# Kernel tuning notes

Measured on AMD Instinct MI355X. Metric: run time of the kernel, lower is better.

The kernel has to match this reference:

```python
import jax, jax.numpy as jnp
import numpy as np
import math

N = 4096
D = 256
H = 8
DH = D // H
E_RAND = 131072
EPS = 1e-5


def _layernorm(x, g, b):
    mu = jnp.mean(x, axis=-1, keepdims=True)
    var = jnp.mean((x - mu) ** 2, axis=-1, keepdims=True)
    return (x - mu) * jax.lax.rsqrt(var + EPS) * g + b


def setup_inputs() -> dict:
    key = jax.random.key(0)
    ks = jax.random.split(key, 16)
    s = 1.0 / math.sqrt(D)
    x = jax.random.normal(ks[0], (N, D), dtype=jnp.float32)
    src = jax.random.randint(ks[1], (E_RAND,), 0, N)
    dst = jax.random.randint(ks[2], (E_RAND,), 0, N)
    loop = jnp.arange(N)
    edge_index = jnp.stack([jnp.concatenate([src, loop]),
                            jnp.concatenate([dst, loop])]).astype(jnp.int64)
    def lin(k):
        return jax.random.normal(k, (D, D), dtype=jnp.float32) * s
    return {
        "x": x,
        "edge_index": edge_index,
        "Wq": lin(ks[3]), "bq": jnp.zeros((D,), jnp.float32),
        "Wk": lin(ks[4]), "bk": jnp.zeros((D,), jnp.float32),
        "Wv": lin(ks[5]), "bv": jnp.zeros((D,), jnp.float32),
        "Wo": lin(ks[6]), "bo": jnp.zeros((D,), jnp.float32),
        "g1": jnp.ones((D,), jnp.float32), "b1": jnp.zeros((D,), jnp.float32),
        "g2": jnp.ones((D,), jnp.float32), "b2": jnp.zeros((D,), jnp.float32),
        "Wm1": jax.random.normal(ks[7], (D, 2 * D), jnp.float32) * s,
        "bm1": jnp.zeros((2 * D,), jnp.float32),
        "Wm2": jax.random.normal(ks[8], (2 * D, D), jnp.float32) * (1.0 / math.sqrt(2 * D)),
        "bm2": jnp.zeros((D,), jnp.float32),
    }


def reference(x, edge_index, Wq, bq, Wk, bk, Wv, bv, Wo, bo,
              g1, b1, g2, b2, Wm1, bm1, Wm2, bm2):
    scale = 1.0 / math.sqrt(DH)
    h = _layernorm(x, g1, b1)
    # [N, D] -> [H, N, DH]
    q = (h @ Wq + bq).reshape(N, H, DH).transpose(1, 0, 2)
    k = (h @ Wk + bk).reshape(N, H, DH).transpose(1, 0, 2)
    v = (h @ Wv + bv).reshape(N, H, DH).transpose(1, 0, 2)
    att = jnp.einsum('hnd,hmd->hnm', q, k) * scale  # [H, N, N]
    # mask: True everywhere except edges (edge positions are attended)
    mask = jnp.ones((N, N), dtype=bool).at[edge_index[0], edge_index[1]].set(False)
    att = jnp.where(mask[None, :, :], -jnp.inf, att)
    att = jax.nn.softmax(att, axis=-1)
    y = jnp.einsum('hnm,hmd->hnd', att, v)  # [H, N, DH]
    y = y.transpose(1, 0, 2).reshape(N, D)
    x = x + (y @ Wo + bo)
    h2 = _layernorm(x, g2, b2)
    x = x + (jax.nn.gelu(h2 @ Wm1 + bm1, approximate=False) @ Wm2 + bm2)
    return x
```

## Files before the change

kernel.cpp:

```cpp
#include <hip/hip_runtime.h>
#include <hip/hip_bf16.h>

#define N_NODES 4096
#define D_MODEL 256
#define NWORDS 128
#define CAP 96

typedef __attribute__((ext_vector_type(8))) short short8;
typedef __attribute__((ext_vector_type(4))) short short4v;
typedef __attribute__((ext_vector_type(4))) float f32x4;

__device__ __forceinline__ unsigned short f2b(float f) {
    unsigned u = __float_as_uint(f);
    return (unsigned short)((u + 0x7FFFu + ((u >> 16) & 1u)) >> 16);
}
__device__ __forceinline__ float b2f(unsigned short u) {
    return __uint_as_float((unsigned)u << 16);
}

__global__ __launch_bounds__(256) void prep_kernel(const float* __restrict__ Wq,
        const float* __restrict__ Wk, const float* __restrict__ Wv,
        const float* __restrict__ Wo, const float* __restrict__ Wm1,
        const float* __restrict__ Wm2, unsigned short* __restrict__ wbf,
        uint4* __restrict__ bitmap, const int* __restrict__ ei,
        int* __restrict__ flag, const float* __restrict__ x,
        const float* __restrict__ g1, const float* __restrict__ b1,
        unsigned short* __restrict__ h) {
    int b = blockIdx.x, t = threadIdx.x;
    if (b < 2048) {
        int e = b * 256 + t;
        const float* W; int base, K, M;
        if (e < 262144) {
            int r = e >> 16;
            W = (r == 0) ? Wq : (r == 1) ? Wk : (r == 2) ? Wv : Wo;
            base = r << 16; K = 256; M = 256;
        } else if (e < 393216) { W = Wm1; base = 262144; K = 256; M = 512; }
        else                   { W = Wm2; base = 393216; K = 512; M = 256; }
        int i = e - base;
        int m = i / K, k = i - m * K;
        wbf[e] = f2b(W[k * M + m]);
    } else if (b < 2560) {
        bitmap[(size_t)(b - 2048) * 256 + t] = uint4{0, 0, 0, 0};
    } else if (b == 2560) {
        if (t == 0) {
            int is64 = 1;
            for (int i = 1; i < 128; i += 2)
                if (ei[i] != 0) { is64 = 0; break; }
            *flag = is64;
        }
    } else {
        int row = b - 2561;
        float v = x[row * D_MODEL + t];
        __shared__ float red[4];
        float s = v;
        #pragma unroll
        for (int off = 32; off; off >>= 1) s += __shfl_down(s, off, 64);
        if ((t & 63) == 0) red[t >> 6] = s;
        __syncthreads();
        float mu = (red[0] + red[1] + red[2] + red[3]) * (1.0f / 256.0f);
        __syncthreads();
        float d = v - mu;
        float s2 = d * d;
        #pragma unroll
        for (int off = 32; off; off >>= 1) s2 += __shfl_down(s2, off, 64);
        if ((t & 63) == 0) red[t >> 6] = s2;
        __syncthreads();
        float var = (red[0] + red[1] + red[2] + red[3]) * (1.0f / 256.0f);
        h[row * D_MODEL + t] = f2b(d * rsqrtf(var + 1e-5f) * g1[t] + b1[t]);
    }
}

template <int K, int MODE, bool LNA, bool STATS>
__global__ __launch_bounds__(512) void gemm_bf16(const unsigned short* __restrict__ A,
        const float* __restrict__ Af, const float* __restrict__ psum,
        const float* __restrict__ psum2, const float* __restrict__ lng,
        const float* __restrict__ lnb, const unsigned short* __restrict__ BT,
        const float* __restrict__ bias, const float* __restrict__ bias_k,
        const float* __restrict__ bias_v, const float* __restrict__ R,
        float* __restrict__ Cf, unsigned short* __restrict__ Cb,
        unsigned short* __restrict__ Ck, unsigned short* __restrict__ Cv,
        float* __restrict__ opsum, float* __restrict__ opsum2, int M,
        const int* __restrict__ ei, int E, const int* __restrict__ flag,
        unsigned* __restrict__ bitmap, int nadj) {
    int tid = threadIdx.x;
    if (MODE == 3 && (int)blockIdx.x < nadj) {
        int e = (int)blockIdx.x * 512 + tid;
        if (e < E) {
            int n, m;
            if (*flag) { n = ei[2 * e]; m = ei[2 * (E + e)]; }
            else       { n = ei[e];     m = ei[E + e]; }
            atomicOr(&bitmap[n * NWORDS + (m >> 5)], 1u << (m & 31));
        }
        return;
    }
    __shared__ unsigned short Asm[64][72];
    __shared__ unsigned short Bsm[64][72];
    __shared__ float psA[64][2], psA2[64][2];
    __shared__ float muS[64], invS[64];

    int bx2  = (MODE == 3) ? ((int)blockIdx.x - nadj) : 0;
    int brow = (MODE == 3) ? ((bx2 & 63) << 6) : ((int)blockIdx.x << 6);
    int by   = (MODE == 3) ? (bx2 >> 6) : (int)blockIdx.y;
    int bcol = by << 6;
    int wid = tid >> 6, lane = tid & 63;
    int wr = wid >> 1, wc = wid & 1;
    int l15 = lane & 15, lhi = lane >> 4;
    int r0 = tid >> 3, c0 = (tid & 7) << 3;

    float mu_r = 0.f, inv_r = 0.f;
    if (LNA) {
        if (tid < 64) {
            float4 s4 = ((const float4*)psum)[brow + tid];
            float4 q4 = ((const float4*)psum2)[brow + tid];
            float S  = s4.x + s4.y + s4.z + s4.w;
            float S2 = q4.x + q4.y + q4.z + q4.w;
            float mu = S * (1.0f / 256.0f);
            muS[tid] = mu;
            invS[tid] = rsqrtf(S2 * (1.0f / 256.0f) - mu * mu + 1e-5f);
        }
        __syncthreads();
        mu_r = muS[r0]; inv_r = invS[r0];
    }

    const unsigned short* Bp = BT + (size_t)(bcol + r0) * K + c0;
    f32x4 acc[2] = {};
    short8 areg;
    float4 xa, xb, ga, gb, ba, bb;
    if (LNA) {
        const float* Xp = Af + (size_t)(brow + r0) * 256 + c0;
        xa = *(const float4*)(Xp);
        xb = *(const float4*)(Xp + 4);
        ga = *(const float4*)(lng + c0); gb = *(const float4*)(lng + c0 + 4);
        ba = *(const float4*)(lnb + c0); bb = *(const float4*)(lnb + c0 + 4);
    } else {
        areg = *(const short8*)(A + (size_t)(brow + r0) * K + c0);
    }
    short8 breg = *(const short8*)(Bp);

    #pragma unroll
    for (int k0 = 0; k0 < K; k0 += 64) {
        if (LNA) {
            float xv[8] = {xa.x, xa.y, xa.z, xa.w, xb.x, xb.y, xb.z, xb.w};
            float gv[8] = {ga.x, ga.y, ga.z, ga.w, gb.x, gb.y, gb.z, gb.w};
            float bv[8] = {ba.x, ba.y, ba.z, ba.w, bb.x, bb.y, bb.z, bb.w};
            short8 o;
            #pragma unroll
            for (int j = 0; j < 8; ++j)
                o[j] = (short)f2b((xv[j] - mu_r) * inv_r * gv[j] + bv[j]);
            *(short8*)&Asm[r0][c0] = o;
        } else {
            *(short8*)&Asm[r0][c0] = areg;
        }
        *(short8*)&Bsm[r0][c0] = breg;
        __syncthreads();
        if (k0 + 64 < K) {
            if (LNA) {
                const float* Xp = Af + (size_t)(brow + r0) * 256 + k0 + 64 + c0;
                xa = *(const float4*)(Xp);
                xb = *(const float4*)(Xp + 4);
                ga = *(const float4*)(lng + k0 + 64 + c0);
                gb = *(const float4*)(lng + k0 + 64 + c0 + 4);
                ba = *(const float4*)(lnb + k0 + 64 + c0);
                bb = *(const float4*)(lnb + k0 + 64 + c0 + 4);
            } else {
                areg = *(const short8*)(A + (size_t)(brow + r0) * K + k0 + 64 + c0);
            }
            breg = *(const short8*)(Bp + k0 + 64);
        }
        #pragma unroll
        for (int ks = 0; ks < 2; ++ks) {
            int kc = ks * 32 + lhi * 8;
            short8 a_0 = *(const short8*)&Asm[wr * 16 + l15][kc];
            short8 b_0 = *(const short8*)&Bsm[wc * 32 + l15][kc];
            short8 b_1 = *(const short8*)&Bsm[wc * 32 + 16 + l15][kc];
            acc[0] = __builtin_amdgcn_mfma_f32_16x16x32_bf16(a_0, b_0, acc[0], 0, 0, 0);
            acc[1] = __builtin_amdgcn_mfma_f32_16x16x32_bf16(a_0, b_1, acc[1], 0, 0, 0);
        }
        __syncthreads();
    }

    float cs[2][4];
    #pragma unroll
    for (int sn = 0; sn < 2; ++sn) {
        int col = bcol + wc * 32 + sn * 16 + l15;
        float bs;
        if (MODE == 3)
            bs = (col < 256) ? bias[col]
               : (col < 512) ? bias_k[col - 256] : bias_v[col - 512];
        else
            bs = bias[col];
        #pragma unroll
        for (int r = 0; r < 4; ++r) {
            int row = brow + wr * 16 + lhi * 4 + r;
            float c = acc[sn][r] + bs;
            if (MODE == 1) {
                c = 0.5f * c * (1.0f + erff(c * 0.70710678118654752f));
                Cb[(size_t)row * M + col] = f2b(c);
            } else if (MODE == 2) {
                c += R[(size_t)row * M + col];
                Cf[(size_t)row * M + col] = c;
            } else if (MODE == 3) {
                int part = col >> 8, cc = col & 255;
                unsigned short* dst = (part == 0) ? Cb : (part == 1) ? Ck : Cv;
                dst[(((size_t)(cc >> 5) * N_NODES + row) << 5) + (cc & 31)] = f2b(c);
            } else {
                Cb[(size_t)row * M + col] = f2b(c);
            }
            if (STATS) cs[sn][r] = c;
        }
    }
    if (STATS) {
        #pragma unroll
        for (int r = 0; r < 4; ++r) {
            float s  = cs[0][r] + cs[1][r];
            float s2 = cs[0][r] * cs[0][r] + cs[1][r] * cs[1][r];
            #pragma unroll
            for (int off = 1; off < 16; off <<= 1) {
                s  += __shfl_xor(s, off, 64);
                s2 += __shfl_xor(s2, off, 64);
            }
            if (l15 == 0) {
                int rl = wr * 16 + lhi * 4 + r;
                psA[rl][wc] = s; psA2[rl][wc] = s2;
            }
        }
        __syncthreads();
        if (tid < 64) {
            opsum [(size_t)(brow + tid) * 4 + by] = psA[tid][0] + psA[tid][1];
            opsum2[(size_t)(brow + tid) * 4 + by] = psA2[tid][0] + psA2[tid][1];
        }
    }
}

#define TRLOAD(dst_, OFF_) \
    asm volatile("ds_read_b64_tr_b16 %0, %1 offset:" #OFF_ \
                 : "=v"(dst_) : "v"(trbase))
#define PVSTEP(tv_, b_) { \
    float4 pv = *(const float4*)&pArr[g][4 * (b_)]; \
    acc = fmaf(pv.x, b2f((unsigned short)tv_[0]), acc); \
    acc = fmaf(pv.y, b2f((unsigned short)tv_[1]), acc); \
    acc = fmaf(pv.z, b2f((unsigned short)tv_[2]), acc); \
    acc = fmaf(pv.w, b2f((unsigned short)tv_[3]), acc); }

__global__ __launch_bounds__(256) void attn_kernel(const unsigned short* __restrict__ qh,
        const unsigned short* __restrict__ kh, const unsigned short* __restrict__ vh,
        const unsigned* __restrict__ bitmap, unsigned short* __restrict__ y) {
    int bid = blockIdx.x, tid = threadIdx.x;
    int h = bid & 7, oct = bid >> 3;
    int g = tid >> 5, lane = tid & 31;
    int n = oct * 8 + g;
    __shared__ int sIdx[8][CAP];
    __shared__ unsigned short Vst[8][2176];
    __shared__ float pArr[8][64];

    const unsigned short* qp = qh + (((size_t)h * N_NODES + n) << 5);
    float qreg[32];
    #pragma unroll
    for (int i = 0; i < 4; ++i) {
        short8 q8 = *(const short8*)(qp + i * 8);
        #pragma unroll
        for (int j = 0; j < 8; ++j) qreg[i * 8 + j] = b2f((unsigned short)q8[j]);
    }

    uint4 w4 = ((const uint4*)(bitmap + (size_t)n * NWORDS))[lane];
    unsigned words[4] = {w4.x, w4.y, w4.z, w4.w};
    int pc = __popc(w4.x) + __popc(w4.y) + __popc(w4.z) + __popc(w4.w);
    int pre = pc;
    #pragma unroll
    for (int off = 1; off < 32; off <<= 1) {
        int u = __shfl_up(pre, off, 32);
        if (lane >= off) pre += u;
    }
    int c = __shfl(pre, 31, 32);
    int off = pre - pc;
    #pragma unroll
    for (int i = 0; i < 4; ++i) {
        unsigned word = words[i];
        int wbase = ((lane << 2) + i) << 5;
        while (word) {
            int bit = __ffs(word) - 1;
            word &= word - 1;
            if (off < CAP) sIdx[g][off] = wbase + bit;
            ++off;
        }
    }
    c = min(c, CAP);
    for (int i = c + lane; i < 64; i += 32) sIdx[g][i] = 0;
    __syncthreads();

    int idx_a = sIdx[g][lane], idx_b = sIdx[g][lane + 32];
    const size_t hb = (size_t)h * N_NODES << 5;

    const unsigned short* va = vh + hb + ((size_t)idx_a << 5);
    const unsigned short* vb = vh + hb + ((size_t)idx_b << 5);
    short8 va0 = *(const short8*)(va);      short8 va1 = *(const short8*)(va + 8);
    short8 va2 = *(const short8*)(va + 16); short8 va3 = *(const short8*)(va + 24);
    short8 vb0 = *(const short8*)(vb);      short8 vb1 = *(const short8*)(vb + 8);
    short8 vb2 = *(const short8*)(vb + 16); short8 vb3 = *(const short8*)(vb + 24);

    const unsigned short* ka = kh + hb + ((size_t)idx_a << 5);
    const unsigned short* kb = kh + hb + ((size_t)idx_b << 5);
    short8 ka0 = *(const short8*)(ka);      short8 ka1 = *(const short8*)(ka + 8);
    short8 ka2 = *(const short8*)(ka + 16); short8 ka3 = *(const short8*)(ka + 24);
    short8 kb0 = *(const short8*)(kb);      short8 kb1 = *(const short8*)(kb + 8);
    short8 kb2 = *(const short8*)(kb + 16); short8 kb3 = *(const short8*)(kb + 24);

    {
        unsigned short* vr = &Vst[g][(lane >> 2) * 136 + (lane & 3) * 16];
        *(short8*)(vr + 0)  = va0;
        *(short8*)(vr + 8)  = va1;
        *(short8*)(vr + 64) = va2;
        *(short8*)(vr + 72) = va3;
        unsigned short* vr2 = vr + 8 * 136;
        *(short8*)(vr2 + 0)  = vb0;
        *(short8*)(vr2 + 8)  = vb1;
        *(short8*)(vr2 + 64) = vb2;
        *(short8*)(vr2 + 72) = vb3;
    }

    float da0 = 0.f, da1 = 0.f, db0 = 0.f, db1 = 0.f;
    #pragma unroll
    for (int e = 0; e < 8; ++e) {
        da0 = fmaf(qreg[e],      b2f((unsigned short)ka0[e]), da0);
        da1 = fmaf(qreg[8 + e],  b2f((unsigned short)ka1[e]), da1);
        da0 = fmaf(qreg[16 + e], b2f((unsigned short)ka2[e]), da0);
        da1 = fmaf(qreg[24 + e], b2f((unsigned short)ka3[e]), da1);
        db0 = fmaf(qreg[e],      b2f((unsigned short)kb0[e]), db0);
        db1 = fmaf(qreg[8 + e],  b2f((unsigned short)kb1[e]), db1);
        db0 = fmaf(qreg[16 + e], b2f((unsigned short)kb2[e]), db0);
        db1 = fmaf(qreg[24 + e], b2f((unsigned short)kb3[e]), db1);
    }
    const float sc = 0.17677669529663687f;
    float s_a = (lane < c)      ? (da0 + da1) * sc : -INFINITY;
    float s_b = (lane + 32 < c) ? (db0 + db1) * sc : -INFINITY;

    float bm = fmaxf(s_a, s_b);
    #pragma unroll
    for (int o2 = 16; o2; o2 >>= 1) bm = fmaxf(bm, __shfl_xor(bm, o2, 32));
    float p_a = (lane < c)      ? __expf(s_a - bm) : 0.0f;
    float p_b = (lane + 32 < c) ? __expf(s_b - bm) : 0.0f;
    float S = p_a + p_b;
    #pragma unroll
    for (int o2 = 16; o2; o2 >>= 1) S += __shfl_xor(S, o2, 32);
    pArr[g][lane] = p_a;
    pArr[g][lane + 32] = p_b;

    unsigned trbase = (unsigned)(uintptr_t)(&Vst[g][0])
                    + ((unsigned)(lane >> 4) << 7) + ((unsigned)(lane & 15) << 3);
    asm volatile("s_waitcnt lgkmcnt(0)" ::: "memory");
    short4v t0, t1, t2, t3, t4, t5, t6, t7, t8, t9, t10, t11, t12, t13, t14, t15;
    TRLOAD(t0, 0);     TRLOAD(t1, 272);  TRLOAD(t2, 544);  TRLOAD(t3, 816);
    TRLOAD(t4, 1088);  TRLOAD(t5, 1360); TRLOAD(t6, 1632); TRLOAD(t7, 1904);
    TRLOAD(t8, 2176);  TRLOAD(t9, 2448); TRLOAD(t10, 2720); TRLOAD(t11, 2992);
    TRLOAD(t12, 3264); TRLOAD(t13, 3536); TRLOAD(t14, 3808); TRLOAD(t15, 4080);
    asm volatile("s_waitcnt lgkmcnt(0)" ::: "memory");
    __builtin_amdgcn_sched_barrier(0);

    float acc = 0.0f;
    PVSTEP(t0, 0)   PVSTEP(t1, 1)   PVSTEP(t2, 2)   PVSTEP(t3, 3)
    PVSTEP(t4, 4)   PVSTEP(t5, 5)   PVSTEP(t6, 6)   PVSTEP(t7, 7)
    PVSTEP(t8, 8)   PVSTEP(t9, 9)   PVSTEP(t10, 10) PVSTEP(t11, 11)
    PVSTEP(t12, 12) PVSTEP(t13, 13) PVSTEP(t14, 14) PVSTEP(t15, 15)

    if (c > 64) {
        float m_run = bm;
        for (int b0 = 64; b0 < c; b0 += 32) {
            int j = b0 + lane;
            float s = -INFINITY;
            if (j < c) {
                const unsigned short* kp = kh + hb + ((size_t)sIdx[g][j] << 5);
                float d = 0.0f;
                #pragma unroll
                for (int i = 0; i < 4; ++i) {
                    short8 k8 = *(const short8*)(kp + i * 8);
                    #pragma unroll
                    for (int e = 0; e < 8; ++e)
                        d = fmaf(qreg[i * 8 + e], b2f((unsigned short)k8[e]), d);
                }
                s = d * sc;
            }
            float bm2 = s;
            #pragma unroll
            for (int o2 = 16; o2; o2 >>= 1) bm2 = fmaxf(bm2, __shfl_xor(bm2, o2, 32));
            float newM = fmaxf(m_run, bm2);
            float p = (j < c) ? __expf(s - newM) : 0.0f;
            float bs = p;
            #pragma unroll
            for (int o2 = 16; o2; o2 >>= 1) bs += __shfl_xor(bs, o2, 32);
            float scale = __expf(m_run - newM);
            S = S * scale + bs;
            acc *= scale;
            int lim = min(32, c - b0);
            const unsigned short* vbase = vh + hb + lane;
            for (int jj = 0; jj < lim; ++jj) {
                float pj = __shfl(p, jj, 32);
                acc = fmaf(pj, b2f(vbase[(size_t)sIdx[g][b0 + jj] << 5]), acc);
            }
            m_run = newM;
        }
    }
    y[(size_t)n * 256 + h * 32 + lane] = f2b(acc / S);
}

extern "C" void kernel_launch(void* const* d_in, const int* in_sizes, int n_in,
                              void* d_out, int out_size, void* d_ws, size_t ws_size,
                              hipStream_t stream) {
    const float* x   = (const float*)d_in[0];
    const int*   ei  = (const int*)d_in[1];
    const float* Wq  = (const float*)d_in[2];  const float* bq  = (const float*)d_in[3];
    const float* Wk  = (const float*)d_in[4];  const float* bk  = (const float*)d_in[5];
    const float* Wv  = (const float*)d_in[6];  const float* bv  = (const float*)d_in[7];
    const float* Wo  = (const float*)d_in[8];  const float* bo  = (const float*)d_in[9];
    const float* g1  = (const float*)d_in[10]; const float* b1  = (const float*)d_in[11];
    const float* g2  = (const float*)d_in[12]; const float* b2  = (const float*)d_in[13];
    const float* Wm1 = (const float*)d_in[14]; const float* bm1 = (const float*)d_in[15];
    const float* Wm2 = (const float*)d_in[16]; const float* bm2 = (const float*)d_in[17];
    float* out = (float*)d_out;
    int E = in_sizes[1] / 2;
    int nadj = (E + 511) / 512;

    char* WS = (char*)d_ws;
    const size_t MB = 1u << 20;
    unsigned*       bitmap = (unsigned*)WS;
    int*            flag   = (int*)(WS + 2 * MB);
    float*          psum   = (float*)(WS + 2 * MB + 4096);
    float*          psum2  = (float*)(WS + 2 * MB + 4096 + 65536);
    unsigned short* wbf    = (unsigned short*)(WS + 3 * MB);
    unsigned short* y      = (unsigned short*)(WS + 4 * MB);
    float*          x1     = (float*)(WS + 6 * MB);
    unsigned short* m1     = (unsigned short*)(WS + 10 * MB);
    unsigned short* h      = (unsigned short*)(WS + 14 * MB);
    unsigned short* qh     = (unsigned short*)(WS + 16 * MB);
    unsigned short* kh     = (unsigned short*)(WS + 18 * MB);
    unsigned short* vh     = (unsigned short*)(WS + 20 * MB);

    const unsigned short* WTqkv = wbf;
    const unsigned short* WTo   = wbf + 196608;
    const unsigned short* WTm1  = wbf + 262144;
    const unsigned short* WTm2  = wbf + 393216;

    prep_kernel<<<6657, 256, 0, stream>>>(Wq, Wk, Wv, Wo, Wm1, Wm2, wbf,
                                          (uint4*)bitmap, ei, flag, x, g1, b1, h);
    gemm_bf16<256, 3, false, false><<<nadj + 768, 512, 0, stream>>>(h, nullptr,
            nullptr, nullptr, nullptr, nullptr, WTqkv, bq, bk, bv, nullptr,
            nullptr, qh, kh, vh, nullptr, nullptr, 768, ei, E, flag, bitmap, nadj);
    attn_kernel<<<N_NODES, 256, 0, stream>>>(qh, kh, vh, bitmap, y);
    gemm_bf16<256, 2, false, true><<<dim3(64, 4), 512, 0, stream>>>(y, nullptr,
            nullptr, nullptr, nullptr, nullptr, WTo, bo, nullptr, nullptr, x,
            x1, nullptr, nullptr, nullptr, psum, psum2, 256, nullptr, 0, nullptr, nullptr, 0);
    gemm_bf16<256, 1, true, false><<<dim3(64, 8), 512, 0, stream>>>(nullptr, x1,
            psum, psum2, g2, b2, WTm1, bm1, nullptr, nullptr, nullptr,
            nullptr, m1, nullptr, nullptr, nullptr, nullptr, 512, nullptr, 0, nullptr, nullptr, 0);
    gemm_bf16<512, 2, false, false><<<dim3(64, 4), 512, 0, stream>>>(m1, nullptr,
            nullptr, nullptr, nullptr, nullptr, WTm2, bm2, nullptr, nullptr, x1,
            out, nullptr, nullptr, nullptr, nullptr, nullptr, 256, nullptr, 0, nullptr, nullptr, 0);
}
```

Baseline: 70.30 us.

## Tile weight transpose via LDS, add BM=128 GEMM tiles, prescale V by probabilities

Weight conversion now transposes 64x64 tiles through shared memory with coalesced float4 reads and short8 writes, replacing the strided per-element gather. The GEMM gains a BM template parameter, and the QKV and MLP1 launches use 128-row tiles so each B tile is reused across twice as many rows, with half as many blocks. In attention, V rows are multiplied by their softmax probability and packed back to bf16 before the transposed LDS reads, so the P·V step becomes plain sums. This drops the pArr shared buffer but rounds p*v to bf16, adding a small precision loss.

```diff
diff --git a/kernel.cpp b/kernel.cpp
--- a/kernel.cpp
+++ b/kernel.cpp
@@ -16,6 +16,19 @@
 }
 __device__ __forceinline__ float b2f(unsigned short u) {
     return __uint_as_float((unsigned)u << 16);
+}
+__device__ __forceinline__ unsigned pk2(float lo, float hi) {
+    unsigned r;
+    asm("v_cvt_pk_bf16_f32 %0, %1, %2" : "=v"(r) : "v"(lo), "v"(hi));
+    return r;
+}
+__device__ __forceinline__ uint4 scale8(short8 v, float p) {
+    uint4 r;
+    r.x = pk2(b2f((unsigned short)v[0]) * p, b2f((unsigned short)v[1]) * p);
+    r.y = pk2(b2f((unsigned short)v[2]) * p, b2f((unsigned short)v[3]) * p);
+    r.z = pk2(b2f((unsigned short)v[4]) * p, b2f((unsigned short)v[5]) * p);
+    r.w = pk2(b2f((unsigned short)v[6]) * p, b2f((unsigned short)v[7]) * p);
+    return r;
 }
 
 __global__ __launch_bounds__(256) void prep_kernel(const float* __restrict__ Wq,
@@ -27,21 +40,34 @@
         const float* __restrict__ g1, const float* __restrict__ b1,
         unsigned short* __restrict__ h) {
     int b = blockIdx.x, t = threadIdx.x;
-    if (b < 2048) {
-        int e = b * 256 + t;
-        const float* W; int base, K, M;
-        if (e < 262144) {
-            int r = e >> 16;
-            W = (r == 0) ? Wq : (r == 1) ? Wk : (r == 2) ? Wv : Wo;
-            base = r << 16; K = 256; M = 256;
-        } else if (e < 393216) { W = Wm1; base = 262144; K = 256; M = 512; }
-        else                   { W = Wm2; base = 393216; K = 512; M = 256; }
-        int i = e - base;
-        int m = i / K, k = i - m * K;
-        wbf[e] = f2b(W[k * M + m]);
-    } else if (b < 2560) {
-        bitmap[(size_t)(b - 2048) * 256 + t] = uint4{0, 0, 0, 0};
-    } else if (b == 2560) {
+    if (b < 128) {
+        const float* W; int base, K, M, kt, mt;
+        if (b < 64)      { int r = b >> 4; W = (r == 0) ? Wq : (r == 1) ? Wk : (r == 2) ? Wv : Wo;
+                           base = r << 16; K = 256; M = 256; kt = (b & 15) >> 2; mt = b & 3; }
+        else if (b < 96) { W = Wm1; base = 262144; K = 256; M = 512; kt = (b - 64) >> 3; mt = (b - 64) & 7; }
+        else             { W = Wm2; base = 393216; K = 512; M = 256; kt = (b - 96) >> 2; mt = (b - 96) & 3; }
+        __shared__ unsigned short Lt[64][66];
+        #pragma unroll
+        for (int i = 0; i < 4; ++i) {
+            int lin = i * 256 + t;
+            int r = lin >> 4, c4 = (lin & 15) << 2;
+            float4 v = *(const float4*)&W[(size_t)(kt * 64 + r) * M + mt * 64 + c4];
+            Lt[r][c4 + 0] = f2b(v.x); Lt[r][c4 + 1] = f2b(v.y);
+            Lt[r][c4 + 2] = f2b(v.z); Lt[r][c4 + 3] = f2b(v.w);
+        }
+        __syncthreads();
+        #pragma unroll
+        for (int i = 0; i < 2; ++i) {
+            int lin = i * 256 + t;
+            int mr = lin >> 3, kc = (lin & 7) << 3;
+            short8 o;
+            #pragma unroll
+            for (int e = 0; e < 8; ++e) o[e] = (short)Lt[kc + e][mr];
+            *(short8*)&wbf[base + (size_t)(mt * 64 + mr) * K + kt * 64 + kc] = o;
+        }
+    } else if (b < 640) {
+        bitmap[(size_t)(b - 128) * 256 + t] = uint4{0, 0, 0, 0};
+    } else if (b == 640) {
         if (t == 0) {
             int is64 = 1;
             for (int i = 1; i < 128; i += 2)
@@ -49,7 +75,7 @@
             *flag = is64;
         }
     } else {
-        int row = b - 2561;
+        int row = b - 641;
         float v = x[row * D_MODEL + t];
         __shared__ float red[4];
         float s = v;
@@ -70,7 +96,7 @@
     }
 }
 
-template <int K, int MODE, bool LNA, bool STATS>
+template <int K, int BM, int MODE, bool LNA, bool STATS>
 __global__ __launch_bounds__(512) void gemm_bf16(const unsigned short* __restrict__ A,
         const float* __restrict__ Af, const float* __restrict__ psum,
         const float* __restrict__ psum2, const float* __restrict__ lng,
@@ -82,6 +108,8 @@
         float* __restrict__ opsum, float* __restrict__ opsum2, int M,
         const int* __restrict__ ei, int E, const int* __restrict__ flag,
         unsigned* __restrict__ bitmap, int nadj) {
+    constexpr int MR = BM / 64;
+    constexpr int NRB = 4096 / BM;
     int tid = threadIdx.x;
     if (MODE == 3 && (int)blockIdx.x < nadj) {
         int e = (int)blockIdx.x * 512 + tid;
@@ -93,23 +121,23 @@
         }
         return;
     }
-    __shared__ unsigned short Asm[64][72];
+    __shared__ unsigned short Asm[BM][72];
     __shared__ unsigned short Bsm[64][72];
     __shared__ float psA[64][2], psA2[64][2];
-    __shared__ float muS[64], invS[64];
+    __shared__ float muS[BM], invS[BM];
 
     int bx2  = (MODE == 3) ? ((int)blockIdx.x - nadj) : 0;
-    int brow = (MODE == 3) ? ((bx2 & 63) << 6) : ((int)blockIdx.x << 6);
-    int by   = (MODE == 3) ? (bx2 >> 6) : (int)blockIdx.y;
+    int brow = (MODE == 3) ? ((bx2 % NRB) * BM) : ((int)blockIdx.x * BM);
+    int by   = (MODE == 3) ? (bx2 / NRB) : (int)blockIdx.y;
     int bcol = by << 6;
     int wid = tid >> 6, lane = tid & 63;
     int wr = wid >> 1, wc = wid & 1;
     int l15 = lane & 15, lhi = lane >> 4;
     int r0 = tid >> 3, c0 = (tid & 7) << 3;
 
-    float mu_r = 0.f, inv_r = 0.f;
+    float mu_r[MR], inv_r[MR];
     if (LNA) {
-        if (tid < 64) {
+        if (tid < BM) {
             float4 s4 = ((const float4*)psum)[brow + tid];
             float4 q4 = ((const float4*)psum2)[brow + tid];
             float S  = s4.x + s4.y + s4.z + s4.w;
@@ -119,96 +147,118 @@
             invS[tid] = rsqrtf(S2 * (1.0f / 256.0f) - mu * mu + 1e-5f);
         }
         __syncthreads();
-        mu_r = muS[r0]; inv_r = invS[r0];
+        #pragma unroll
+        for (int m = 0; m < MR; ++m) { mu_r[m] = muS[r0 + m * 64]; inv_r[m] = invS[r0 + m * 64]; }
     }
 
     const unsigned short* Bp = BT + (size_t)(bcol + r0) * K + c0;
-    f32x4 acc[2] = {};
-    short8 areg;
-    float4 xa, xb, ga, gb, ba, bb;
+    f32x4 acc[MR][2] = {};
+    short8 areg[MR];
+    float4 xa[MR], xb[MR], ga, gb, ba, bb;
     if (LNA) {
-        const float* Xp = Af + (size_t)(brow + r0) * 256 + c0;
-        xa = *(const float4*)(Xp);
-        xb = *(const float4*)(Xp + 4);
+        #pragma unroll
+        for (int m = 0; m < MR; ++m) {
+            const float* Xp = Af + (size_t)(brow + r0 + m * 64) * 256 + c0;
+            xa[m] = *(const float4*)(Xp);
+            xb[m] = *(const float4*)(Xp + 4);
+        }
         ga = *(const float4*)(lng + c0); gb = *(const float4*)(lng + c0 + 4);
         ba = *(const float4*)(lnb + c0); bb = *(const float4*)(lnb + c0 + 4);
     } else {
-        areg = *(const short8*)(A + (size_t)(brow + r0) * K + c0);
+        #pragma unroll
+        for (int m = 0; m < MR; ++m)
+            areg[m] = *(const short8*)(A + (size_t)(brow + r0 + m * 64) * K + c0);
     }
     short8 breg = *(const short8*)(Bp);
 
     #pragma unroll
     for (int k0 = 0; k0 < K; k0 += 64) {
         if (LNA) {
-            float xv[8] = {xa.x, xa.y, xa.z, xa.w, xb.x, xb.y, xb.z, xb.w};
-            float gv[8] = {ga.x, ga.y, ga.z, ga.w, gb.x, gb.y, gb.z, gb.w};
-            float bv[8] = {ba.x, ba.y, ba.z, ba.w, bb.x, bb.y, bb.z, bb.w};
-            short8 o;
-            #pragma unroll
-            for (int j = 0; j < 8; ++j)
-                o[j] = (short)f2b((xv[j] - mu_r) * inv_r * gv[j] + bv[j]);
-            *(short8*)&Asm[r0][c0] = o;
+            #pragma unroll
+            for (int m = 0; m < MR; ++m) {
+                float xv[8] = {xa[m].x, xa[m].y, xa[m].z, xa[m].w,
+                               xb[m].x, xb[m].y, xb[m].z, xb[m].w};
+                float gv[8] = {ga.x, ga.y, ga.z, ga.w, gb.x, gb.y, gb.z, gb.w};
+                float bv[8] = {ba.x, ba.y, ba.z, ba.w, bb.x, bb.y, bb.z, bb.w};
+                short8 o;
+                #pragma unroll
+                for (int j = 0; j < 8; ++j)
+                    o[j] = (short)f2b((xv[j] - mu_r[m]) * inv_r[m] * gv[j] + bv[j]);
+                *(short8*)&Asm[r0 + m * 64][c0] = o;
+            }
         } else {
-            *(short8*)&Asm[r0][c0] = areg;
+            #pragma unroll
+            for (int m = 0; m < MR; ++m)
+                *(short8*)&Asm[r0 + m * 64][c0] = areg[m];
         }
         *(short8*)&Bsm[r0][c0] = breg;
         __syncthreads();
         if (k0 + 64 < K) {
             if (LNA) {
-                const float* Xp = Af + (size_t)(brow + r0) * 256 + k0 + 64 + c0;
-                xa = *(const float4*)(Xp);
-                xb = *(const float4*)(Xp + 4);
+                #pragma unroll
+                for (int m = 0; m < MR; ++m) {
+                    const float* Xp = Af + (size_t)(brow + r0 + m * 64) * 256 + k0 + 64 + c0;
+                    xa[m] = *(const float4*)(Xp);
+                    xb[m] = *(const float4*)(Xp + 4);
+                }
                 ga = *(const float4*)(lng + k0 + 64 + c0);
                 gb = *(const float4*)(lng + k0 + 64 + c0 + 4);
                 ba = *(const float4*)(lnb + k0 + 64 + c0);
                 bb = *(const float4*)(lnb + k0 + 64 + c0 + 4);
             } else {
-                areg = *(const short8*)(A + (size_t)(brow + r0) * K + k0 + 64 + c0);
+                #pragma unroll
+                for (int m = 0; m < MR; ++m)
+                    areg[m] = *(const short8*)(A + (size_t)(brow + r0 + m * 64) * K + k0 + 64 + c0);
             }
             breg = *(const short8*)(Bp + k0 + 64);
         }
         #pragma unroll
         for (int ks = 0; ks < 2; ++ks) {
             int kc = ks * 32 + lhi * 8;
-            short8 a_0 = *(const short8*)&Asm[wr * 16 + l15][kc];
             short8 b_0 = *(const short8*)&Bsm[wc * 32 + l15][kc];
             short8 b_1 = *(const short8*)&Bsm[wc * 32 + 16 + l15][kc];
-            acc[0] = __builtin_amdgcn_mfma_f32_16x16x32_bf16(a_0, b_0, acc[0], 0, 0, 0);
-            acc[1] = __builtin_amdgcn_mfma_f32_16x16x32_bf16(a_0, b_1, acc[1], 0, 0, 0);
+            #pragma unroll
+            for (int sm = 0; sm < MR; ++sm) {
+                short8 a_s = *(const short8*)&Asm[wr * 16 * MR + sm * 16 + l15][kc];
+                acc[sm][0] = __builtin_amdgcn_mfma_f32_16x16x32_bf16(a_s, b_0, acc[sm][0], 0, 0, 0);
+                acc[sm][1] = __builtin_amdgcn_mfma_f32_16x16x32_bf16(a_s, b_1, acc[sm][1], 0, 0, 0);
+            }
         }
         __syncthreads();
     }
 
     float cs[2][4];
     #pragma unroll
-    for (int sn = 0; sn < 2; ++sn) {
-        int col = bcol + wc * 32 + sn * 16 + l15;
-        float bs;
-        if (MODE == 3)
-            bs = (col < 256) ? bias[col]
-               : (col < 512) ? bias_k[col - 256] : bias_v[col - 512];
-        else
-            bs = bias[col];
-        #pragma unroll
-        for (int r = 0; r < 4; ++r) {
-            int row = brow + wr * 16 + lhi * 4 + r;
-            float c = acc[sn][r] + bs;
-            if (MODE == 1) {
-                c = 0.5f * c * (1.0f + erff(c * 0.70710678118654752f));
-                Cb[(size_t)row * M + col] = f2b(c);
-            } else if (MODE == 2) {
-                c += R[(size_t)row * M + col];
-                Cf[(size_t)row * M + col] = c;
-            } else if (MODE == 3) {
-                int part = col >> 8, cc = col & 255;
-                unsigned short* dst = (part == 0) ? Cb : (part == 1) ? Ck : Cv;
-                dst[(((size_t)(cc >> 5) * N_NODES + row) << 5) + (cc & 31)] = f2b(c);
-            } else {
-                Cb[(size_t)row * M + col] = f2b(c);
-            }
-            if (STATS) cs[sn][r] = c;
-        }
-    }
+    for (int sm = 0; sm < MR; ++sm)
+        #pragma unroll
+        for (int sn = 0; sn < 2; ++sn) {
+            int col = bcol + wc * 32 + sn * 16 + l15;
+            float bs;
+            if (MODE == 3)
+                bs = (col < 256) ? bias[col]
+                   : (col < 512) ? bias_k[col - 256] : bias_v[col - 512];
+            else
+                bs = bias[col];
+            #pragma unroll
+            for (int r = 0; r < 4; ++r) {
+                int row = brow + wr * 16 * MR + sm * 16 + lhi * 4 + r;
+                float c = acc[sm][sn][r] + bs;
+                if (MODE == 1) {
+                    c = 0.5f * c * (1.0f + erff(c * 0.70710678118654752f));
+                    Cb[(size_t)row * M + col] = f2b(c);
+                } else if (MODE == 2) {
+                    c += R[(size_t)row * M + col];
+                    Cf[(size_t)row * M + col] = c;
+                } else if (MODE == 3) {
+                    int part = col >> 8, cc = col & 255;
+                    unsigned short* dst = (part == 0) ? Cb : (part == 1) ? Ck : Cv;
+                    dst[(((size_t)(cc >> 5) * N_NODES + row) << 5) + (cc & 31)] = f2b(c);
+                } else {
+                    Cb[(size_t)row * M + col] = f2b(c);
+                }
+                if (STATS) cs[sn][r] = c;
+            }
+        }
     if (STATS) {
         #pragma unroll
         for (int r = 0; r < 4; ++r) {
@@ -235,12 +285,9 @@
 #define TRLOAD(dst_, OFF_) \
     asm volatile("ds_read_b64_tr_b16 %0, %1 offset:" #OFF_ \
                  : "=v"(dst_) : "v"(trbase))
-#define PVSTEP(tv_, b_) { \
-    float4 pv = *(const float4*)&pArr[g][4 * (b_)]; \
-    acc = fmaf(pv.x, b2f((unsigned short)tv_[0]), acc); \
-    acc = fmaf(pv.y, b2f((unsigned short)tv_[1]), acc); \
-    acc = fmaf(pv.z, b2f((unsigned short)tv_[2]), acc); \
-    acc = fmaf(pv.w, b2f((unsigned short)tv_[3]), acc); }
+#define PVSUM(tv_) { \
+    acc0 += b2f((unsigned short)tv_[0]); acc1 += b2f((unsigned short)tv_[1]); \
+    acc0 += b2f((unsigned short)tv_[2]); acc1 += b2f((unsigned short)tv_[3]); }
 
 __global__ __launch_bounds__(256) void attn_kernel(const unsigned short* __restrict__ qh,
         const unsigned short* __restrict__ kh, const unsigned short* __restrict__ vh,
@@ -251,7 +298,6 @@
     int n = oct * 8 + g;
     __shared__ int sIdx[8][CAP];
     __shared__ unsigned short Vst[8][2176];
-    __shared__ float pArr[8][64];
 
     const unsigned short* qp = qh + (((size_t)h * N_NODES + n) << 5);
     float qreg[32];
@@ -304,19 +350,6 @@
     short8 ka2 = *(const short8*)(ka + 16); short8 ka3 = *(const short8*)(ka + 24);
     short8 kb0 = *(const short8*)(kb);      short8 kb1 = *(const short8*)(kb + 8);
     short8 kb2 = *(const short8*)(kb + 16); short8 kb3 = *(const short8*)(kb + 24);
-
-    {
-        unsigned short* vr = &Vst[g][(lane >> 2) * 136 + (lane & 3) * 16];
-        *(short8*)(vr + 0)  = va0;
-        *(short8*)(vr + 8)  = va1;
-        *(short8*)(vr + 64) = va2;
-        *(short8*)(vr + 72) = va3;
-        unsigned short* vr2 = vr + 8 * 136;
-        *(short8*)(vr2 + 0)  = vb0;
-        *(short8*)(vr2 + 8)  = vb1;
-        *(short8*)(vr2 + 64) = vb2;
-        *(short8*)(vr2 + 72) = vb3;
-    }
 
     float da0 = 0.f, da1 = 0.f, db0 = 0.f, db1 = 0.f;
     #pragma unroll
@@ -342,8 +375,19 @@
     float S = p_a + p_b;
     #pragma unroll
     for (int o2 = 16; o2; o2 >>= 1) S += __shfl_xor(S, o2, 32);
-    pArr[g][lane] = p_a;
-    pArr[g][lane + 32] = p_b;
+
+    {
+        unsigned short* vr = &Vst[g][(lane >> 2) * 136 + (lane & 3) * 16];
+        *(uint4*)(vr + 0)  = scale8(va0, p_a);
+        *(uint4*)(vr + 8)  = scale8(va1, p_a);
+        *(uint4*)(vr + 64) = scale8(va2, p_a);
+        *(uint4*)(vr + 72) = scale8(va3, p_a);
+        unsigned short* vr2 = vr + 8 * 136;
+        *(uint4*)(vr2 + 0)  = scale8(vb0, p_b);
+        *(uint4*)(vr2 + 8)  = scale8(vb1, p_b);
+        *(uint4*)(vr2 + 64) = scale8(vb2, p_b);
+        *(uint4*)(vr2 + 72) = scale8(vb3, p_b);
+    }
 
     unsigned trbase = (unsigned)(uintptr_t)(&Vst[g][0])
                     + ((unsigned)(lane >> 4) << 7) + ((unsigned)(lane & 15) << 3);
@@ -356,11 +400,12 @@
     asm volatile("s_waitcnt lgkmcnt(0)" ::: "memory");
     __builtin_amdgcn_sched_barrier(0);
 
-    float acc = 0.0f;
-    PVSTEP(t0, 0)   PVSTEP(t1, 1)   PVSTEP(t2, 2)   PVSTEP(t3, 3)
-    PVSTEP(t4, 4)   PVSTEP(t5, 5)   PVSTEP(t6, 6)   PVSTEP(t7, 7)
-    PVSTEP(t8, 8)   PVSTEP(t9, 9)   PVSTEP(t10, 10) PVSTEP(t11, 11)
-    PVSTEP(t12, 12) PVSTEP(t13, 13) PVSTEP(t14, 14) PVSTEP(t15, 15)
+    float acc0 = 0.0f, acc1 = 0.0f;
+    PVSUM(t0)  PVSUM(t1)  PVSUM(t2)  PVSUM(t3)
+    PVSUM(t4)  PVSUM(t5)  PVSUM(t6)  PVSUM(t7)
+    PVSUM(t8)  PVSUM(t9)  PVSUM(t10) PVSUM(t11)
+    PVSUM(t12) PVSUM(t13) PVSUM(t14) PVSUM(t15)
+    float acc = acc0 + acc1;
 
     if (c > 64) {
         float m_run = bm;
@@ -439,19 +484,19 @@
     const unsigned short* WTm1  = wbf + 262144;
     const unsigned short* WTm2  = wbf + 393216;
 
-    prep_kernel<<<6657, 256, 0, stream>>>(Wq, Wk, Wv, Wo, Wm1, Wm2, wbf,
+    prep_kernel<<<4737, 256, 0, stream>>>(Wq, Wk, Wv, Wo, Wm1, Wm2, wbf,
                                           (uint4*)bitmap, ei, flag, x, g1, b1, h);
-    gemm_bf16<256, 3, false, false><<<nadj + 768, 512, 0, stream>>>(h, nullptr,
+    gemm_bf16<256, 128, 3, false, false><<<nadj + 384, 512, 0, stream>>>(h, nullptr,
             nullptr, nullptr, nullptr, nullptr, WTqkv, bq, bk, bv, nullptr,
             nullptr, qh, kh, vh, nullptr, nullptr, 768, ei, E, flag, bitmap, nadj);
     attn_kernel<<<N_NODES, 256, 0, stream>>>(qh, kh, vh, bitmap, y);
-    gemm_bf16<256, 2, false, true><<<dim3(64, 4), 512, 0, stream>>>(y, nullptr,
+    gemm_bf16<256, 64, 2, false, true><<<dim3(64, 4), 512, 0, stream>>>(y, nullptr,
             nullptr, nullptr, nullptr, nullptr, WTo, bo, nullptr, nullptr, x,
             x1, nullptr, nullptr, nullptr, psum, psum2, 256, nullptr, 0, nullptr, nullptr, 0);
-    gemm_bf16<256, 1, true, false><<<dim3(64, 8), 512, 0, stream>>>(nullptr, x1,
+    gemm_bf16<256, 128, 1, true, false><<<dim3(32, 8), 512, 0, stream>>>(nullptr, x1,
             psum, psum2, g2, b2, WTm1, bm1, nullptr, nullptr, nullptr,
             nullptr, m1, nullptr, nullptr, nullptr, nullptr, 512, nullptr, 0, nullptr, nullptr, 0);
-    gemm_bf16<512, 2, false, false><<<dim3(64, 4), 512, 0, stream>>>(m1, nullptr,
+    gemm_bf16<512, 64, 2, false, false><<<dim3(64, 4), 512, 0, stream>>>(m1, nullptr,
             nullptr, nullptr, nullptr, nullptr, WTm2, bm2, nullptr, nullptr, x1,
             out, nullptr, nullptr, nullptr, nullptr, nullptr, 256, nullptr, 0, nullptr, nullptr, 0);
 }
```

After: 71.47 us. Within noise of the previous version (+1.7%).
